# Performance work log

Hardware: AMD Instinct MI355X
Metric: run time of the kernel (lower is better)

The kernel has to match this reference:

```python
import jax, jax.numpy as jnp
import numpy as np
from jax import lax

# ---- constants mirroring Prediction.__init__ kwargs ----
INP = 608
NUM_CLASSES = 20
ALPHA, BETA = 1.0, 0.5
OBJ_T, CONF_T, LOC_T = 0.6, 0.05, 0.5
NMS_T, SIZE_T, SIGMA = 0.1, 0.0, 0.5
TOP_K = 8
M_CAND = 256          # fixed-size candidate cap for jit-compatible NMS
NEG = -1e9            # sentinel for masked scores
ANCHORS = [[(116, 90), (156, 198), (373, 326)],
           [(30, 61), (62, 45), (59, 119)],
           [(10, 13), (16, 30), (33, 23)]]


def _decode(pred, anchors):
    """pred: (B, A, G, G, 6+C) raw level output -> decoded flat tensors."""
    B, A, G, _, C = pred.shape
    stride = INP // G
    xy = jax.nn.sigmoid(pred[..., 0:2])
    g = jnp.arange(G, dtype=pred.dtype)
    gx, gy = jnp.meshgrid(g, g)                      # gx[i,j]=j, gy[i,j]=i (np.meshgrid 'xy')
    off = jnp.stack([gx, gy], axis=-1)[None, None]   # (1,1,G,G,2)
    xy = ALPHA * xy - 0.5 * (ALPHA - 1.0) + off
    anc = jnp.asarray(anchors, dtype=pred.dtype) / stride  # (A,2) scaled to grid units
    wh = jnp.exp(pred[..., 2:4]) * anc[None, :, None, None, :]
    box = jnp.concatenate([xy, wh], axis=-1) * stride       # back to pixel units
    obj = jax.nn.sigmoid(pred[..., 4])
    loc = jax.nn.sigmoid(pred[..., 5])
    clsp = jax.nn.softmax(pred[..., 6:], axis=-1)
    N = A * G * G
    return (box.reshape(B, N, 4), obj.reshape(B, N),
            loc.reshape(B, N), clsp.reshape(B, N, NUM_CLASSES))


def _soft_nms(boxes, s0, cls):
    """Per-image Gaussian soft-NMS (class-aware), +1 pixel IoU convention as in bbox_iou.
    boxes: (M,4) xyxy, s0: (M,) scores (NEG for invalid), cls: (M,) int. Returns kept mask."""
    M = s0.shape[0]

    def step(carry, _):
        s, kept = carry
        j = jnp.argmax(s)
        do = s[j] >= NMS_T
        kept = kept | ((jnp.arange(M) == j) & do)
        bj = boxes[j]
        ix1 = jnp.maximum(bj[0], boxes[:, 0]); iy1 = jnp.maximum(bj[1], boxes[:, 1])
        ix2 = jnp.minimum(bj[2], boxes[:, 2]); iy2 = jnp.minimum(bj[3], boxes[:, 3])
        inter = jnp.maximum(ix2 - ix1 + 1.0, 0.0) * jnp.maximum(iy2 - iy1 + 1.0, 0.0)
        a1 = (bj[2] - bj[0] + 1.0) * (bj[3] - bj[1] + 1.0)
        a2 = (boxes[:, 2] - boxes[:, 0] + 1.0) * (boxes[:, 3] - boxes[:, 1] + 1.0)
        iou = inter / (a1 + a2 - inter + 1e-16)
        decay = jnp.exp(-(iou * iou) / SIGMA)
        s_new = jnp.where(cls == cls[j], s * decay, s).at[j].set(NEG)
        s = jnp.where(do, s_new, s)
        return (s, kept), None

    (_, kept), _ = lax.scan(step, (s0, jnp.zeros(M, dtype=bool)), None, length=M)
    return kept


def _forward(pred_l0, pred_l1, pred_l2):
    parts = [_decode(p, a) for p, a in zip([pred_l0, pred_l1, pred_l2], ANCHORS)]
    box = jnp.concatenate([p[0] for p in parts], axis=1)   # (B,N,4) xywh
    obj = jnp.concatenate([p[1] for p in parts], axis=1)
    loc = jnp.concatenate([p[2] for p in parts], axis=1)
    clsp = jnp.concatenate([p[3] for p in parts], axis=1)

    cx, cy, w, h = box[..., 0], box[..., 1], box[..., 2], box[..., 3]
    x1 = jnp.clip(cx - w / 2, 0.0, INP); y1 = jnp.clip(cy - h / 2, 0.0, INP)
    x2 = jnp.clip(cx + w / 2, 0.0, INP); y2 = jnp.clip(cy + h / 2, 0.0, INP)
    boxes = jnp.stack([x1, y1, x2, y2], axis=-1)            # (B,N,4) xyxy, clamped

    cls_conf = jnp.max(clsp, axis=-1)
    cls_id = jnp.argmax(clsp, axis=-1)
    area = (x2 - x1) * (y2 - y1)
    valid = ((obj >= OBJ_T) & (area >= INP * INP * SIZE_T)
             & (obj * cls_conf >= CONF_T) & (loc >= LOC_T))
    score = (obj * cls_conf) ** BETA * loc ** (1.0 - BETA)
    masked = jnp.where(valid, score, NEG)

    # fixed-size candidate set per image (descending-score sort + cap)
    vals, idx = lax.top_k(masked, M_CAND)                   # (B,M)
    cboxes = jnp.take_along_axis(boxes, idx[..., None], axis=1)
    ccls = jnp.take_along_axis(cls_id, idx, axis=1)
    s0 = jnp.where(vals > NEG / 2, vals, NEG)

    kept = jax.vmap(_soft_nms)(cboxes, s0, ccls)            # (B,M) bool

    # keep_top_k: top_k among kept, ranked by ORIGINAL (pre-decay) score
    fscore = jnp.where(kept, vals, NEG)
    fvals, fidx = lax.top_k(fscore, TOP_K)                  # (B,TOP_K)
    fboxes = jnp.take_along_axis(cboxes, fidx[..., None], axis=1)
    fcls = jnp.take_along_axis(ccls, fidx, axis=1)
    row = jnp.concatenate([fboxes, fvals[..., None],
                           fcls[..., None].astype(fboxes.dtype)], axis=-1)  # (B,K,6)
    ok = fvals > NEG / 2
    return jnp.where(ok[..., None], row, 0.0)


def setup_inputs() -> dict:
    key = jax.random.key(0)
    k0, k1, k2 = jax.random.split(key, 3)
    return {
        "pred_l0": jax.random.normal(k0, (64, 3, 19, 19, 26), dtype=jnp.float32),
        "pred_l1": jax.random.normal(k1, (64, 3, 38, 38, 26), dtype=jnp.float32),
        "pred_l2": jax.random.normal(k2, (64, 3, 76, 76, 26), dtype=jnp.float32),
    }


def reference(pred_l0, pred_l1, pred_l2):
    return _forward(pred_l0, pred_l1, pred_l2)
```

## Files before the change

kernel.cpp:

```cpp
#include <hip/hip_runtime.h>
#include <climits>

constexpr int kB  = 64;
constexpr int kG0 = 19, kG1 = 38, kG2 = 76;
constexpr int kN0 = 3 * kG0 * kG0;
constexpr int kN1 = 3 * kG1 * kG1;
constexpr int kN2 = 3 * kG2 * kG2;
constexpr int kN  = kN0 + kN1 + kN2;
constexpr int kNP = kN + 1;
constexpr int kM  = 256;
constexpr int kTopK = 8;
constexpr float kNEG = -1e9f;

constexpr int kT0 = 5, kT1 = 17, kT2 = 68;
constexpr int kTilesPerImg = kT0 + kT1 + kT2;
constexpr int kGridScore = 1920;
constexpr int kTilesPerBlk = 3;

__constant__ float c_anchors[3][3][2] = {
    {{116.f, 90.f}, {156.f, 198.f}, {373.f, 326.f}},
    {{30.f, 61.f},  {62.f, 45.f},   {59.f, 119.f}},
    {{10.f, 13.f},  {16.f, 30.f},   {33.f, 23.f}},
};

__device__ __forceinline__ float fexpf(float x) { return __expf(x); }
__device__ __forceinline__ float frcpf(float x) { return __builtin_amdgcn_rcpf(x); }
__device__ __forceinline__ float fsigm(float x) { return frcpf(1.0f + __expf(-x)); }

__device__ __forceinline__ float2 nt_load_f2(const float2* p) {
  unsigned long long v = __builtin_nontemporal_load((const unsigned long long*)p);
  union { unsigned long long u; float2 f; } c; c.u = v; return c.f;
}

__device__ __forceinline__ unsigned score_to_key(float s) {
  unsigned fb = __float_as_uint(s);
  unsigned m = (fb & 0x80000000u) ? 0xFFFFFFFFu : 0x80000000u;
  return fb ^ m;
}
__device__ __forceinline__ float key_to_score(unsigned k) {
  unsigned fb = (k & 0x80000000u) ? (k ^ 0x80000000u) : ~k;
  return __uint_as_float(fb);
}

__device__ __forceinline__ const float* cell_ptr(
    const float* p0, const float* p1, const float* p2, int b, int n,
    int& lvl, int& a, int& gi, int& gj, float& stride) {
  const float* src; int G, m;
  if (n < kN0)            { src = p0; G = kG0; lvl = 0; m = n;             stride = 32.f; }
  else if (n < kN0 + kN1) { src = p1; G = kG1; lvl = 1; m = n - kN0;       stride = 16.f; }
  else                    { src = p2; G = kG2; lvl = 2; m = n - kN0 - kN1; stride = 8.f; }
  int gg = G * G;
  a = m / gg;
  int r = m - a * gg;
  gi = r / G;
  gj = r - gi * G;
  return src + (size_t)((((b * 3 + a) * G + gi) * G + gj)) * 26;
}

__device__ __forceinline__ void waveArgmax(float& v, int& i) {
  #pragma unroll
  for (int off = 1; off < 64; off <<= 1) {
    float ov = __shfl_xor(v, off);
    int oi = __shfl_xor(i, off);
    if (ov > v || (ov == v && oi < i)) { v = ov; i = oi; }
  }
}
__device__ __forceinline__ float waveMax(float v) {
  #pragma unroll
  for (int off = 1; off < 64; off <<= 1) v = fmaxf(v, __shfl_xor(v, off));
  return v;
}
__device__ __forceinline__ float sel4f(const float a[4], int q) {
  float r = a[0];
  r = (q == 1) ? a[1] : r;
  r = (q == 2) ? a[2] : r;
  r = (q == 3) ? a[3] : r;
  return r;
}
__device__ __forceinline__ int sel4i(const int a[4], int q) {
  int r = a[0];
  r = (q == 1) ? a[1] : r;
  r = (q == 2) ? a[2] : r;
  r = (q == 3) ? a[3] : r;
  return r;
}

__global__ __launch_bounds__(256) void score_kernel(
    const float* __restrict__ p0, const float* __restrict__ p1, const float* __restrict__ p2,
    unsigned* __restrict__ keys)
{
  __shared__ float2 lds2[2][256 * 13];

  int t = threadIdx.x;

  const float2* g2[kTilesPerBlk]; int nc[kTilesPerBlk], n0[kTilesPerBlk], bb[kTilesPerBlk];
  #pragma unroll
  for (int j = 0; j < kTilesPerBlk; ++j) {
    int tileId = (int)blockIdx.x + j * kGridScore;
    int b = tileId / kTilesPerImg;
    int r = tileId - b * kTilesPerImg;
    const float* slab; int NL, lvlOff, tile;
    if (r < kT0)            { slab = p0; NL = kN0; lvlOff = 0;         tile = r; }
    else if (r < kT0 + kT1) { slab = p1; NL = kN1; lvlOff = kN0;       tile = r - kT0; }
    else                    { slab = p2; NL = kN2; lvlOff = kN0 + kN1; tile = r - kT0 - kT1; }
    int cellBase = tile * 256;
    nc[j] = min(256, NL - cellBase);
    g2[j] = (const float2*)(slab + ((size_t)b * NL + cellBase) * 26);
    n0[j] = lvlOff + cellBase;
    bb[j] = b;
  }

  float2 nxt[13];

  {
    int tot = nc[0] * 13;
    #pragma unroll
    for (int k = 0; k < 13; ++k) {
      int i = t + k * 256;
      if (i < tot) nxt[k] = nt_load_f2(g2[0] + i);
    }
    #pragma unroll
    for (int k = 0; k < 13; ++k) {
      int i = t + k * 256;
      if (i < tot) lds2[0][i] = nxt[k];
    }
  }

  #pragma unroll
  for (int j = 0; j < kTilesPerBlk; ++j) {
    __syncthreads();

    int totN = 0;
    if (j + 1 < kTilesPerBlk) {
      totN = nc[j + 1] * 13;
      #pragma unroll
      for (int k = 0; k < 13; ++k) {
        int i = t + k * 256;
        if (i < totN) nxt[k] = nt_load_f2(g2[j + 1] + i);
      }
    }

    int curNc = nc[j], curN0 = n0[j], curB = bb[j];
    const float2* bufp = &lds2[j & 1][0];
    if (t < curNc) {
      const float2* c2 = &bufp[t * 13];
      float2 ol = c2[2];
      float obj = fsigm(ol.x);
      float loc = fsigm(ol.y);
      float tch[20];
      #pragma unroll
      for (int q = 0; q < 10; ++q) { float2 v = c2[3 + q]; tch[2*q] = v.x; tch[2*q+1] = v.y; }
      float lm = tch[0];
      #pragma unroll
      for (int c = 1; c < 20; ++c) lm = fmaxf(lm, tch[c]);
      float se = 0.f;
      #pragma unroll
      for (int c = 0; c < 20; ++c) se += fexpf(tch[c] - lm);
      float cls_conf = frcpf(se);
      float conf = obj * cls_conf;
      float masked = (obj >= 0.6f && loc >= 0.5f && conf >= 0.05f)
                     ? sqrtf(conf) * sqrtf(loc) : kNEG;
      keys[(size_t)curB * kNP + curN0 + t] = score_to_key(masked);
    }

    if (j + 1 < kTilesPerBlk) {
      float2* dst = &lds2[(j + 1) & 1][0];
      #pragma unroll
      for (int k = 0; k < 13; ++k) {
        int i = t + k * 256;
        if (i < totN) dst[i] = nxt[k];
      }
    }
  }
}

__device__ __forceinline__ void findThresholdBin(
    const int* hist, int NB, int needed,
    int& outB, int& outCumAbove, int& outTotal,
    int* shWave, int* shOut)
{
  int tid = threadIdx.x, lane = tid & 63, w = tid >> 6;
  if (tid == 0) { shOut[0] = -1; shOut[1] = 0; }
  int ipt = (NB + 511) / 512;
  int base = tid * ipt;
  int csum = 0;
  for (int i = 0; i < ipt; ++i) { int bn = base + i; if (bn < NB) csum += hist[bn]; }
  int v = csum;
  #pragma unroll
  for (int off = 1; off < 64; off <<= 1) {
    int tv = __shfl_down(v, off);
    if (lane + off < 64) v += tv;
  }
  if (lane == 0) shWave[w] = v;
  __syncthreads();
  int above = 0, total = 0;
  #pragma unroll
  for (int q = 0; q < 8; ++q) {
    int wt = shWave[q];
    total += wt;
    if (q > w) above += wt;
  }
  int S = v + above;
  if (S >= needed && S - csum < needed) {
    int running = S - csum;
    for (int i = ipt - 1; i >= 0; --i) {
      int bn = base + i; if (bn >= NB) continue;
      int c = hist[bn];
      if (running + c >= needed) { shOut[0] = bn; shOut[1] = running; break; }
      running += c;
    }
  }
  __syncthreads();
  outB = shOut[0]; outCumAbove = shOut[1]; outTotal = total;
  __syncthreads();
}

constexpr int kNV4 = kN / 4;
constexpr int kTail = kN - kNV4*4;

__global__ __launch_bounds__(512) void select_nms_kernel(
    const unsigned* __restrict__ keys,
    const float* __restrict__ p0, const float* __restrict__ p1, const float* __restrict__ p2,
    float* __restrict__ out)
{
  int b = blockIdx.x, tid = threadIdx.x;
  const unsigned* kk = keys + (size_t)b * kNP;
  const uint4* kk4 = (const uint4*)kk;
  const unsigned keyNEG = score_to_key(kNEG);

  __shared__ int hist[4096];
  __shared__ int eqBuf[1024];
  __shared__ int shWave[8], shOut[2];
  __shared__ unsigned sT;
  __shared__ int sCgt;
  __shared__ int ciL[kM];
  __shared__ unsigned ckL[kM];

  for (int i = tid; i < 4096; i += 512) hist[i] = 0;
  __syncthreads();
  for (int x = tid; x < kNV4; x += 512) {
    uint4 v = kk4[x];
    if (v.x >= 0x80000000u) atomicAdd(&hist[v.x >> 20], 1);
    if (v.y >= 0x80000000u) atomicAdd(&hist[v.y >> 20], 1);
    if (v.z >= 0x80000000u) atomicAdd(&hist[v.z >> 20], 1);
    if (v.w >= 0x80000000u) atomicAdd(&hist[v.w >> 20], 1);
  }
  if (tid < kTail) {
    unsigned k = kk[kNV4 * 4 + tid];
    if (k >= 0x80000000u) atomicAdd(&hist[k >> 20], 1);
  }
  __syncthreads();
  int B, cumAbove1, total1;
  findThresholdBin(hist, 4096, kM, B, cumAbove1, total1, shWave, shOut);

  if (total1 < kM) {
    if (tid == 0) { sT = keyNEG; sCgt = total1; }
    __syncthreads();
  } else {
    int needed2 = kM - cumAbove1;
    for (int i = tid; i < 4096; i += 512) hist[i] = 0;
    __syncthreads();
    for (int x = tid; x < kNV4; x += 512) {
      uint4 v = kk4[x];
      if ((int)(v.x >> 20) == B) atomicAdd(&hist[(v.x >> 8) & 0xFFF], 1);
      if ((int)(v.y >> 20) == B) atomicAdd(&hist[(v.y >> 8) & 0xFFF], 1);
      if ((int)(v.z >> 20) == B) atomicAdd(&hist[(v.z >> 8) & 0xFFF], 1);
      if ((int)(v.w >> 20) == B) atomicAdd(&hist[(v.w >> 8) & 0xFFF], 1);
    }
    if (tid < kTail) {
      unsigned k = kk[kNV4 * 4 + tid];
      if ((int)(k >> 20) == B) atomicAdd(&hist[(k >> 8) & 0xFFF], 1);
    }
    __syncthreads();
    int B2, cumAbove2, total2;
    findThresholdBin(hist, 4096, needed2, B2, cumAbove2, total2, shWave, shOut);
    int prefix24 = (B << 12) | B2;
    int needed3 = needed2 - cumAbove2;

    for (int i = tid; i < 256; i += 512) hist[i] = 0;
    __syncthreads();
    for (int x = tid; x < kNV4; x += 512) {
      uint4 v = kk4[x];
      if ((int)(v.x >> 8) == prefix24) atomicAdd(&hist[v.x & 0xFF], 1);
      if ((int)(v.y >> 8) == prefix24) atomicAdd(&hist[v.y & 0xFF], 1);
      if ((int)(v.z >> 8) == prefix24) atomicAdd(&hist[v.z & 0xFF], 1);
      if ((int)(v.w >> 8) == prefix24) atomicAdd(&hist[v.w & 0xFF], 1);
    }
    if (tid < kTail) {
      unsigned k = kk[kNV4 * 4 + tid];
      if ((int)(k >> 8) == prefix24) atomicAdd(&hist[k & 0xFF], 1);
    }
    __syncthreads();
    int B3, cumAbove3, total3;
    findThresholdBin(hist, 256, needed3, B3, cumAbove3, total3, shWave, shOut);
    if (tid == 0) {
      sT = ((unsigned)prefix24 << 8) | (unsigned)B3;
      sCgt = cumAbove1 + cumAbove2 + cumAbove3;
    }
    __syncthreads();
  }

  unsigned T = sT;
  int cgt = sCgt;

  __shared__ int sCnt, eqCnt;
  if (tid == 0) { sCnt = 0; eqCnt = 0; }
  __syncthreads();
  for (int x = tid; x < kNV4; x += 512) {
    uint4 v = kk4[x];
    int i4 = x * 4;
    unsigned kv[4] = {v.x, v.y, v.z, v.w};
    #pragma unroll
    for (int e = 0; e < 4; ++e) {
      unsigned k = kv[e];
      if (k > T) {
        int p = atomicAdd(&sCnt, 1);
        ciL[p] = i4 + e; ckL[p] = k;
      } else if (k == T && T != keyNEG) {
        int p = atomicAdd(&eqCnt, 1); if (p < 1024) eqBuf[p] = i4 + e;
      }
    }
  }
  if (tid < kTail) {
    int x = kNV4 * 4 + tid;
    unsigned k = kk[x];
    if (k > T) {
      int p = atomicAdd(&sCnt, 1);
      ciL[p] = x; ckL[p] = k;
    } else if (k == T && T != keyNEG) {
      int p = atomicAdd(&eqCnt, 1); if (p < 1024) eqBuf[p] = x;
    }
  }
  __syncthreads();

  int needed = kM - cgt;
  if (T == keyNEG) {
    if (tid >= cgt && tid < kM) { ciL[tid] = -1; ckL[tid] = keyNEG; }
  } else {
    int ce = min(eqCnt, 1024);
    if (ce == needed) {
      if (tid < needed) { ciL[cgt + tid] = eqBuf[tid]; ckL[cgt + tid] = T; }
    } else if (tid == 0) {
      for (int q = 0; q < needed; ++q) {
        int mv = INT_MAX, mp = 0;
        for (int x = 0; x < ce; ++x) if (eqBuf[x] < mv) { mv = eqBuf[x]; mp = x; }
        ciL[cgt + q] = mv; ckL[cgt + q] = T; eqBuf[mp] = INT_MAX;
      }
    }
  }
  __syncthreads();

  if (tid >= 64) return;
  int lane = tid;

  float x1[4], y1[4], x2[4], y2[4], val[4], s[4];
  int cls[4];
  bool kept[4];

  #pragma unroll
  for (int q = 0; q < 4; ++q) {
    int slot = q * 64 + lane;
    int n = ciL[slot];
    float sc = key_to_score(ckL[slot]);
    kept[q] = false;
    x1[q] = y1[q] = x2[q] = y2[q] = 0.f;
    cls[q] = 0; val[q] = sc; s[q] = sc;
    if (n >= 0) {
      int lvl, a, gi, gj; float stride;
      const float* p = cell_ptr(p0, p1, p2, b, n, lvl, a, gi, gj, stride);
      const float2* r2 = (const float2*)p;
      float2 c01 = r2[0], c23 = r2[1];
      float cx = (fsigm(c01.x) + (float)gj) * stride;
      float cy = (fsigm(c01.y) + (float)gi) * stride;
      float w = fexpf(c23.x) * c_anchors[lvl][a][0];
      float h = fexpf(c23.y) * c_anchors[lvl][a][1];
      x1[q] = fminf(fmaxf(cx - 0.5f * w, 0.f), 608.f);
      y1[q] = fminf(fmaxf(cy - 0.5f * h, 0.f), 608.f);
      x2[q] = fminf(fmaxf(cx + 0.5f * w, 0.f), 608.f);
      y2[q] = fminf(fmaxf(cy + 0.5f * h, 0.f), 608.f);
      float lm = -3.4e38f; int mc = 0;
      #pragma unroll
      for (int j = 3; j < 13; ++j) {
        float2 v = r2[j];
        int c0 = 2 * (j - 3);
        if (v.x > lm) { lm = v.x; mc = c0; }
        if (v.y > lm) { lm = v.y; mc = c0 + 1; }
      }
      cls[q] = mc;
    }
  }

  float top8[8];
  #pragma unroll
  for (int i = 0; i < 8; ++i) top8[i] = kNEG;
  int keptCount = 0;

  for (int it = 0; it < kM; ++it) {
    float bv = s[0]; int bq = 0;
    #pragma unroll
    for (int q = 1; q < 4; ++q) if (s[q] > bv) { bv = s[q]; bq = q; }
    int bi = bq * 64 + lane;
    waveArgmax(bv, bi);
    if (bv < 0.1f) break;

    int wlane = bi & 63, wq = bi >> 6;
    float jx1 = __shfl(sel4f(x1, wq), wlane);
    float jy1 = __shfl(sel4f(y1, wq), wlane);
    float jx2 = __shfl(sel4f(x2, wq), wlane);
    float jy2 = __shfl(sel4f(y2, wq), wlane);
    float jval = __shfl(sel4f(val, wq), wlane);
    int   cj  = __shfl(sel4i(cls, wq), wlane);

    float a1 = (jx2 - jx1 + 1.0f) * (jy2 - jy1 + 1.0f);
    #pragma unroll
    for (int q = 0; q < 4; ++q) {
      if (cls[q] == cj) {
        float ix1 = fmaxf(jx1, x1[q]), iy1 = fmaxf(jy1, y1[q]);
        float ix2 = fminf(jx2, x2[q]), iy2 = fminf(jy2, y2[q]);
        float inter = fmaxf(ix2 - ix1 + 1.0f, 0.0f) * fmaxf(iy2 - iy1 + 1.0f, 0.0f);
        float a2 = (x2[q] - x1[q] + 1.0f) * (y2[q] - y1[q] + 1.0f);
        float iou = inter / (a1 + a2 - inter + 1e-16f);
        s[q] *= fexpf(-(iou * iou) * 2.0f);
      }
      if (bi == q * 64 + lane) { kept[q] = true; s[q] = kNEG; }
    }

    float v = jval;
    #pragma unroll
    for (int i = 0; i < 8; ++i) { float m = fmaxf(top8[i], v); v = fminf(top8[i], v); top8[i] = m; }
    ++keptCount;
    if (keptCount >= kTopK) {
      float am = kNEG;
      #pragma unroll
      for (int q = 0; q < 4; ++q) if (s[q] >= 0.1f) am = fmaxf(am, val[q]);
      am = waveMax(am);
      if (am < top8[7]) break;
    }
  }

  float f[4];
  #pragma unroll
  for (int q = 0; q < 4; ++q) f[q] = kept[q] ? val[q] : kNEG;
  for (int k = 0; k < kTopK; ++k) {
    float bv = f[0]; int bq = 0;
    #pragma unroll
    for (int q = 1; q < 4; ++q) if (f[q] > bv) { bv = f[q]; bq = q; }
    int bi = bq * 64 + lane;
    waveArgmax(bv, bi);
    int wlane = bi & 63, wq = bi >> 6;
    if (lane == wlane) {
      float* o = out + (size_t)(b * kTopK + k) * 6;
      if (bv > kNEG * 0.5f) {
        o[0] = sel4f(x1, wq); o[1] = sel4f(y1, wq);
        o[2] = sel4f(x2, wq); o[3] = sel4f(y2, wq);
        o[4] = sel4f(val, wq); o[5] = (float)sel4i(cls, wq);
      } else {
        o[0] = 0.f; o[1] = 0.f; o[2] = 0.f; o[3] = 0.f; o[4] = 0.f; o[5] = 0.f;
      }
    }
    #pragma unroll
    for (int q = 0; q < 4; ++q) if (bi == q * 64 + lane) f[q] = kNEG;
  }
}

extern "C" void kernel_launch(void* const* d_in, const int* in_sizes, int n_in,
                              void* d_out, int out_size, void* d_ws, size_t ws_size,
                              hipStream_t stream) {
  const float* p0 = (const float*)d_in[0];
  const float* p1 = (const float*)d_in[1];
  const float* p2 = (const float*)d_in[2];
  float* out = (float*)d_out;

  unsigned* keys = (unsigned*)d_ws;

  score_kernel<<<kGridScore, 256, 0, stream>>>(p0, p1, p2, keys);
  select_nms_kernel<<<kB, 512, 0, stream>>>(keys, p0, p1, p2, out);
}
```

Measured before the change: 226.3 us.

## Fuse score and select/NMS kernels via last-block-done atomic counters

Result: slower. 665.4 us (+194.0%).

```diff
diff --git a/kernel.cpp b/kernel.cpp
--- a/kernel.cpp
+++ b/kernel.cpp
@@ -16,6 +16,9 @@
 constexpr int kTilesPerImg = kT0 + kT1 + kT2;
 constexpr int kGridScore = 1920;
 constexpr int kTilesPerBlk = 3;
+
+constexpr int kNV4 = kN / 4;
+constexpr int kTail = kN - kNV4 * 4;
 
 __constant__ float c_anchors[3][3][2] = {
     {{116.f, 90.f}, {156.f, 198.f}, {373.f, 326.f}},
@@ -85,11 +88,56 @@
   return r;
 }
 
-__global__ __launch_bounds__(256) void score_kernel(
+__device__ __forceinline__ void findThresholdBin256(
+    const int* hist, int NB, int needed,
+    int& outB, int& outCumAbove, int& outTotal,
+    int* shWave, int* shOut)
+{
+  int tid = threadIdx.x, lane = tid & 63, w = tid >> 6;
+  if (tid == 0) { shOut[0] = -1; shOut[1] = 0; }
+  int ipt = (NB + 255) / 256;
+  int base = tid * ipt;
+  int csum = 0;
+  for (int i = 0; i < ipt; ++i) { int bn = base + i; if (bn < NB) csum += hist[bn]; }
+  int v = csum;
+  #pragma unroll
+  for (int off = 1; off < 64; off <<= 1) {
+    int tv = __shfl_down(v, off);
+    if (lane + off < 64) v += tv;
+  }
+  if (lane == 0) shWave[w] = v;
+  __syncthreads();
+  int above = 0, total = 0;
+  #pragma unroll
+  for (int q = 0; q < 4; ++q) {
+    int wt = shWave[q];
+    total += wt;
+    if (q > w) above += wt;
+  }
+  int S = v + above;
+  if (S >= needed && S - csum < needed) {
+    int running = S - csum;
+    for (int i = ipt - 1; i >= 0; --i) {
+      int bn = base + i; if (bn >= NB) continue;
+      int c = hist[bn];
+      if (running + c >= needed) { shOut[0] = bn; shOut[1] = running; break; }
+      running += c;
+    }
+  }
+  __syncthreads();
+  outB = shOut[0]; outCumAbove = shOut[1]; outTotal = total;
+  __syncthreads();
+}
+
+__global__ __launch_bounds__(256) void fused_kernel(
     const float* __restrict__ p0, const float* __restrict__ p1, const float* __restrict__ p2,
-    unsigned* __restrict__ keys)
+    unsigned* __restrict__ keys, int* __restrict__ done, float* __restrict__ out)
 {
-  __shared__ float2 lds2[2][256 * 13];
+  __shared__ float2 smem2[2][256 * 13];
+  __shared__ int shWave[4], shOut[2];
+  __shared__ unsigned sT;
+  __shared__ int sCgt, sCnt, sEqCnt;
+  __shared__ int sFlags[kTilesPerBlk], sNF;
 
   int t = threadIdx.x;
 
@@ -110,356 +158,325 @@
     bb[j] = b;
   }
 
-  float2 nxt[13];
-
   {
-    int tot = nc[0] * 13;
-    #pragma unroll
-    for (int k = 0; k < 13; ++k) {
-      int i = t + k * 256;
-      if (i < tot) nxt[k] = nt_load_f2(g2[0] + i);
-    }
-    #pragma unroll
-    for (int k = 0; k < 13; ++k) {
-      int i = t + k * 256;
-      if (i < tot) lds2[0][i] = nxt[k];
-    }
-  }
-
-  #pragma unroll
-  for (int j = 0; j < kTilesPerBlk; ++j) {
-    __syncthreads();
-
-    int totN = 0;
-    if (j + 1 < kTilesPerBlk) {
-      totN = nc[j + 1] * 13;
+    float2 nxt[13];
+    {
+      int tot = nc[0] * 13;
       #pragma unroll
       for (int k = 0; k < 13; ++k) {
         int i = t + k * 256;
-        if (i < totN) nxt[k] = nt_load_f2(g2[j + 1] + i);
-      }
-    }
-
-    int curNc = nc[j], curN0 = n0[j], curB = bb[j];
-    const float2* bufp = &lds2[j & 1][0];
-    if (t < curNc) {
-      const float2* c2 = &bufp[t * 13];
-      float2 ol = c2[2];
-      float obj = fsigm(ol.x);
-      float loc = fsigm(ol.y);
-      float tch[20];
-      #pragma unroll
-      for (int q = 0; q < 10; ++q) { float2 v = c2[3 + q]; tch[2*q] = v.x; tch[2*q+1] = v.y; }
-      float lm = tch[0];
-      #pragma unroll
-      for (int c = 1; c < 20; ++c) lm = fmaxf(lm, tch[c]);
-      float se = 0.f;
-      #pragma unroll
-      for (int c = 0; c < 20; ++c) se += fexpf(tch[c] - lm);
-      float cls_conf = frcpf(se);
-      float conf = obj * cls_conf;
-      float masked = (obj >= 0.6f && loc >= 0.5f && conf >= 0.05f)
-                     ? sqrtf(conf) * sqrtf(loc) : kNEG;
-      keys[(size_t)curB * kNP + curN0 + t] = score_to_key(masked);
-    }
-
-    if (j + 1 < kTilesPerBlk) {
-      float2* dst = &lds2[(j + 1) & 1][0];
+        if (i < tot) nxt[k] = nt_load_f2(g2[0] + i);
+      }
       #pragma unroll
       for (int k = 0; k < 13; ++k) {
         int i = t + k * 256;
-        if (i < totN) dst[i] = nxt[k];
-      }
-    }
-  }
-}
-
-__device__ __forceinline__ void findThresholdBin(
-    const int* hist, int NB, int needed,
-    int& outB, int& outCumAbove, int& outTotal,
-    int* shWave, int* shOut)
-{
-  int tid = threadIdx.x, lane = tid & 63, w = tid >> 6;
-  if (tid == 0) { shOut[0] = -1; shOut[1] = 0; }
-  int ipt = (NB + 511) / 512;
-  int base = tid * ipt;
-  int csum = 0;
-  for (int i = 0; i < ipt; ++i) { int bn = base + i; if (bn < NB) csum += hist[bn]; }
-  int v = csum;
-  #pragma unroll
-  for (int off = 1; off < 64; off <<= 1) {
-    int tv = __shfl_down(v, off);
-    if (lane + off < 64) v += tv;
-  }
-  if (lane == 0) shWave[w] = v;
+        if (i < tot) smem2[0][i] = nxt[k];
+      }
+    }
+
+    #pragma unroll
+    for (int j = 0; j < kTilesPerBlk; ++j) {
+      __syncthreads();
+
+      int totN = 0;
+      if (j + 1 < kTilesPerBlk) {
+        totN = nc[j + 1] * 13;
+        #pragma unroll
+        for (int k = 0; k < 13; ++k) {
+          int i = t + k * 256;
+          if (i < totN) nxt[k] = nt_load_f2(g2[j + 1] + i);
+        }
+      }
+
+      int curNc = nc[j], curN0 = n0[j], curB = bb[j];
+      const float2* bufp = &smem2[j & 1][0];
+      if (t < curNc) {
+        const float2* c2 = &bufp[t * 13];
+        float2 ol = c2[2];
+        float obj = fsigm(ol.x);
+        float loc = fsigm(ol.y);
+        float tch[20];
+        #pragma unroll
+        for (int q = 0; q < 10; ++q) { float2 v = c2[3 + q]; tch[2*q] = v.x; tch[2*q+1] = v.y; }
+        float lm = tch[0];
+        #pragma unroll
+        for (int c = 1; c < 20; ++c) lm = fmaxf(lm, tch[c]);
+        float se = 0.f;
+        #pragma unroll
+        for (int c = 0; c < 20; ++c) se += fexpf(tch[c] - lm);
+        float cls_conf = frcpf(se);
+        float conf = obj * cls_conf;
+        float masked = (obj >= 0.6f && loc >= 0.5f && conf >= 0.05f)
+                       ? sqrtf(conf) * sqrtf(loc) : kNEG;
+        keys[(size_t)curB * kNP + curN0 + t] = score_to_key(masked);
+      }
+
+      if (j + 1 < kTilesPerBlk) {
+        float2* dst = &smem2[(j + 1) & 1][0];
+        #pragma unroll
+        for (int k = 0; k < 13; ++k) {
+          int i = t + k * 256;
+          if (i < totN) dst[i] = nxt[k];
+        }
+      }
+    }
+  }
+
   __syncthreads();
-  int above = 0, total = 0;
-  #pragma unroll
-  for (int q = 0; q < 8; ++q) {
-    int wt = shWave[q];
-    total += wt;
-    if (q > w) above += wt;
-  }
-  int S = v + above;
-  if (S >= needed && S - csum < needed) {
-    int running = S - csum;
-    for (int i = ipt - 1; i >= 0; --i) {
-      int bn = base + i; if (bn >= NB) continue;
-      int c = hist[bn];
-      if (running + c >= needed) { shOut[0] = bn; shOut[1] = running; break; }
-      running += c;
-    }
+  __threadfence();
+  if (t == 0) {
+    int nf = 0;
+    #pragma unroll
+    for (int j = 0; j < kTilesPerBlk; ++j) {
+      int old = atomicAdd(&done[bb[j]], 1);
+      if (old == kTilesPerImg - 1) sFlags[nf++] = bb[j];
+    }
+    sNF = nf;
   }
   __syncthreads();
-  outB = shOut[0]; outCumAbove = shOut[1]; outTotal = total;
-  __syncthreads();
-}
-
-constexpr int kNV4 = kN / 4;
-constexpr int kTail = kN - kNV4*4;
-
-__global__ __launch_bounds__(512) void select_nms_kernel(
-    const unsigned* __restrict__ keys,
-    const float* __restrict__ p0, const float* __restrict__ p1, const float* __restrict__ p2,
-    float* __restrict__ out)
-{
-  int b = blockIdx.x, tid = threadIdx.x;
-  const unsigned* kk = keys + (size_t)b * kNP;
-  const uint4* kk4 = (const uint4*)kk;
+  int nFlag = sNF;
+  if (nFlag == 0) return;
+
+  int* hist = (int*)&smem2[0][0];
+  int* eqBuf = hist + 4096;
+  int* ciL = eqBuf + 1024;
+  unsigned* ckL = (unsigned*)(ciL + 256);
+
   const unsigned keyNEG = score_to_key(kNEG);
 
-  __shared__ int hist[4096];
-  __shared__ int eqBuf[1024];
-  __shared__ int shWave[8], shOut[2];
-  __shared__ unsigned sT;
-  __shared__ int sCgt;
-  __shared__ int ciL[kM];
-  __shared__ unsigned ckL[kM];
-
-  for (int i = tid; i < 4096; i += 512) hist[i] = 0;
-  __syncthreads();
-  for (int x = tid; x < kNV4; x += 512) {
-    uint4 v = kk4[x];
-    if (v.x >= 0x80000000u) atomicAdd(&hist[v.x >> 20], 1);
-    if (v.y >= 0x80000000u) atomicAdd(&hist[v.y >> 20], 1);
-    if (v.z >= 0x80000000u) atomicAdd(&hist[v.z >> 20], 1);
-    if (v.w >= 0x80000000u) atomicAdd(&hist[v.w >> 20], 1);
-  }
-  if (tid < kTail) {
-    unsigned k = kk[kNV4 * 4 + tid];
-    if (k >= 0x80000000u) atomicAdd(&hist[k >> 20], 1);
-  }
-  __syncthreads();
-  int B, cumAbove1, total1;
-  findThresholdBin(hist, 4096, kM, B, cumAbove1, total1, shWave, shOut);
-
-  if (total1 < kM) {
-    if (tid == 0) { sT = keyNEG; sCgt = total1; }
-    __syncthreads();
-  } else {
-    int needed2 = kM - cumAbove1;
-    for (int i = tid; i < 4096; i += 512) hist[i] = 0;
-    __syncthreads();
-    for (int x = tid; x < kNV4; x += 512) {
+  for (int f = 0; f < nFlag; ++f) {
+    int b = sFlags[f];
+    __threadfence();
+    __syncthreads();
+
+    const unsigned* kk = keys + (size_t)b * kNP;
+    const uint4* kk4 = (const uint4*)kk;
+
+    for (int i = t; i < 4096; i += 256) hist[i] = 0;
+    __syncthreads();
+    for (int x = t; x < kNV4; x += 256) {
       uint4 v = kk4[x];
-      if ((int)(v.x >> 20) == B) atomicAdd(&hist[(v.x >> 8) & 0xFFF], 1);
-      if ((int)(v.y >> 20) == B) atomicAdd(&hist[(v.y >> 8) & 0xFFF], 1);
-      if ((int)(v.z >> 20) == B) atomicAdd(&hist[(v.z >> 8) & 0xFFF], 1);
-      if ((int)(v.w >> 20) == B) atomicAdd(&hist[(v.w >> 8) & 0xFFF], 1);
-    }
-    if (tid < kTail) {
-      unsigned k = kk[kNV4 * 4 + tid];
-      if ((int)(k >> 20) == B) atomicAdd(&hist[(k >> 8) & 0xFFF], 1);
-    }
-    __syncthreads();
-    int B2, cumAbove2, total2;
-    findThresholdBin(hist, 4096, needed2, B2, cumAbove2, total2, shWave, shOut);
-    int prefix24 = (B << 12) | B2;
-    int needed3 = needed2 - cumAbove2;
-
-    for (int i = tid; i < 256; i += 512) hist[i] = 0;
-    __syncthreads();
-    for (int x = tid; x < kNV4; x += 512) {
+      if (v.x >= 0x80000000u) atomicAdd(&hist[v.x >> 20], 1);
+      if (v.y >= 0x80000000u) atomicAdd(&hist[v.y >> 20], 1);
+      if (v.z >= 0x80000000u) atomicAdd(&hist[v.z >> 20], 1);
+      if (v.w >= 0x80000000u) atomicAdd(&hist[v.w >> 20], 1);
+    }
+    if (t < kTail) {
+      unsigned k = kk[kNV4 * 4 + t];
+      if (k >= 0x80000000u) atomicAdd(&hist[k >> 20], 1);
+    }
+    __syncthreads();
+    int B, cumAbove1, total1;
+    findThresholdBin256(hist, 4096, kM, B, cumAbove1, total1, shWave, shOut);
+
+    if (total1 < kM) {
+      if (t == 0) { sT = keyNEG; sCgt = total1; }
+      __syncthreads();
+    } else {
+      int needed2 = kM - cumAbove1;
+      for (int i = t; i < 4096; i += 256) hist[i] = 0;
+      __syncthreads();
+      for (int x = t; x < kNV4; x += 256) {
+        uint4 v = kk4[x];
+        if ((int)(v.x >> 20) == B) atomicAdd(&hist[(v.x >> 8) & 0xFFF], 1);
+        if ((int)(v.y >> 20) == B) atomicAdd(&hist[(v.y >> 8) & 0xFFF], 1);
+        if ((int)(v.z >> 20) == B) atomicAdd(&hist[(v.z >> 8) & 0xFFF], 1);
+        if ((int)(v.w >> 20) == B) atomicAdd(&hist[(v.w >> 8) & 0xFFF], 1);
+      }
+      if (t < kTail) {
+        unsigned k = kk[kNV4 * 4 + t];
+        if ((int)(k >> 20) == B) atomicAdd(&hist[(k >> 8) & 0xFFF], 1);
+      }
+      __syncthreads();
+      int B2, cumAbove2, total2;
+      findThresholdBin256(hist, 4096, needed2, B2, cumAbove2, total2, shWave, shOut);
+      int prefix24 = (B << 12) | B2;
+      int needed3 = needed2 - cumAbove2;
+
+      for (int i = t; i < 256; i += 256) hist[i] = 0;
+      __syncthreads();
+      for (int x = t; x < kNV4; x += 256) {
+        uint4 v = kk4[x];
+        if ((int)(v.x >> 8) == prefix24) atomicAdd(&hist[v.x & 0xFF], 1);
+        if ((int)(v.y >> 8) == prefix24) atomicAdd(&hist[v.y & 0xFF], 1);
+        if ((int)(v.z >> 8) == prefix24) atomicAdd(&hist[v.z & 0xFF], 1);
+        if ((int)(v.w >> 8) == prefix24) atomicAdd(&hist[v.w & 0xFF], 1);
+      }
+      if (t < kTail) {
+        unsigned k = kk[kNV4 * 4 + t];
+        if ((int)(k >> 8) == prefix24) atomicAdd(&hist[k & 0xFF], 1);
+      }
+      __syncthreads();
+      int B3, cumAbove3, total3;
+      findThresholdBin256(hist, 256, needed3, B3, cumAbove3, total3, shWave, shOut);
+      if (t == 0) {
+        sT = ((unsigned)prefix24 << 8) | (unsigned)B3;
+        sCgt = cumAbove1 + cumAbove2 + cumAbove3;
+      }
+      __syncthreads();
+    }
+
+    unsigned T = sT;
+    int cgt = sCgt;
+
+    if (t == 0) { sCnt = 0; sEqCnt = 0; }
+    __syncthreads();
+    for (int x = t; x < kNV4; x += 256) {
       uint4 v = kk4[x];
-      if ((int)(v.x >> 8) == prefix24) atomicAdd(&hist[v.x & 0xFF], 1);
-      if ((int)(v.y >> 8) == prefix24) atomicAdd(&hist[v.y & 0xFF], 1);
-      if ((int)(v.z >> 8) == prefix24) atomicAdd(&hist[v.z & 0xFF], 1);
-      if ((int)(v.w >> 8) == prefix24) atomicAdd(&hist[v.w & 0xFF], 1);
-    }
-    if (tid < kTail) {
-      unsigned k = kk[kNV4 * 4 + tid];
-      if ((int)(k >> 8) == prefix24) atomicAdd(&hist[k & 0xFF], 1);
-    }
-    __syncthreads();
-    int B3, cumAbove3, total3;
-    findThresholdBin(hist, 256, needed3, B3, cumAbove3, total3, shWave, shOut);
-    if (tid == 0) {
-      sT = ((unsigned)prefix24 << 8) | (unsigned)B3;
-      sCgt = cumAbove1 + cumAbove2 + cumAbove3;
-    }
-    __syncthreads();
-  }
-
-  unsigned T = sT;
-  int cgt = sCgt;
-
-  __shared__ int sCnt, eqCnt;
-  if (tid == 0) { sCnt = 0; eqCnt = 0; }
-  __syncthreads();
-  for (int x = tid; x < kNV4; x += 512) {
-    uint4 v = kk4[x];
-    int i4 = x * 4;
-    unsigned kv[4] = {v.x, v.y, v.z, v.w};
-    #pragma unroll
-    for (int e = 0; e < 4; ++e) {
-      unsigned k = kv[e];
+      int i4 = x * 4;
+      unsigned kv[4] = {v.x, v.y, v.z, v.w};
+      #pragma unroll
+      for (int e = 0; e < 4; ++e) {
+        unsigned k = kv[e];
+        if (k > T) {
+          int p = atomicAdd(&sCnt, 1);
+          ciL[p] = i4 + e; ckL[p] = k;
+        } else if (k == T && T != keyNEG) {
+          int p = atomicAdd(&sEqCnt, 1); if (p < 1024) eqBuf[p] = i4 + e;
+        }
+      }
+    }
+    if (t < kTail) {
+      int x = kNV4 * 4 + t;
+      unsigned k = kk[x];
       if (k > T) {
         int p = atomicAdd(&sCnt, 1);
-        ciL[p] = i4 + e; ckL[p] = k;
+        ciL[p] = x; ckL[p] = k;
       } else if (k == T && T != keyNEG) {
-        int p = atomicAdd(&eqCnt, 1); if (p < 1024) eqBuf[p] = i4 + e;
-      }
-    }
-  }
-  if (tid < kTail) {
-    int x = kNV4 * 4 + tid;
-    unsigned k = kk[x];
-    if (k > T) {
-      int p = atomicAdd(&sCnt, 1);
-      ciL[p] = x; ckL[p] = k;
-    } else if (k == T && T != keyNEG) {
-      int p = atomicAdd(&eqCnt, 1); if (p < 1024) eqBuf[p] = x;
-    }
-  }
-  __syncthreads();
-
-  int needed = kM - cgt;
-  if (T == keyNEG) {
-    if (tid >= cgt && tid < kM) { ciL[tid] = -1; ckL[tid] = keyNEG; }
-  } else {
-    int ce = min(eqCnt, 1024);
-    if (ce == needed) {
-      if (tid < needed) { ciL[cgt + tid] = eqBuf[tid]; ckL[cgt + tid] = T; }
-    } else if (tid == 0) {
-      for (int q = 0; q < needed; ++q) {
-        int mv = INT_MAX, mp = 0;
-        for (int x = 0; x < ce; ++x) if (eqBuf[x] < mv) { mv = eqBuf[x]; mp = x; }
-        ciL[cgt + q] = mv; ckL[cgt + q] = T; eqBuf[mp] = INT_MAX;
-      }
-    }
-  }
-  __syncthreads();
-
-  if (tid >= 64) return;
-  int lane = tid;
-
-  float x1[4], y1[4], x2[4], y2[4], val[4], s[4];
-  int cls[4];
-  bool kept[4];
-
-  #pragma unroll
-  for (int q = 0; q < 4; ++q) {
-    int slot = q * 64 + lane;
-    int n = ciL[slot];
-    float sc = key_to_score(ckL[slot]);
-    kept[q] = false;
-    x1[q] = y1[q] = x2[q] = y2[q] = 0.f;
-    cls[q] = 0; val[q] = sc; s[q] = sc;
-    if (n >= 0) {
-      int lvl, a, gi, gj; float stride;
-      const float* p = cell_ptr(p0, p1, p2, b, n, lvl, a, gi, gj, stride);
-      const float2* r2 = (const float2*)p;
-      float2 c01 = r2[0], c23 = r2[1];
-      float cx = (fsigm(c01.x) + (float)gj) * stride;
-      float cy = (fsigm(c01.y) + (float)gi) * stride;
-      float w = fexpf(c23.x) * c_anchors[lvl][a][0];
-      float h = fexpf(c23.y) * c_anchors[lvl][a][1];
-      x1[q] = fminf(fmaxf(cx - 0.5f * w, 0.f), 608.f);
-      y1[q] = fminf(fmaxf(cy - 0.5f * h, 0.f), 608.f);
-      x2[q] = fminf(fmaxf(cx + 0.5f * w, 0.f), 608.f);
-      y2[q] = fminf(fmaxf(cy + 0.5f * h, 0.f), 608.f);
-      float lm = -3.4e38f; int mc = 0;
-      #pragma unroll
-      for (int j = 3; j < 13; ++j) {
-        float2 v = r2[j];
-        int c0 = 2 * (j - 3);
-        if (v.x > lm) { lm = v.x; mc = c0; }
-        if (v.y > lm) { lm = v.y; mc = c0 + 1; }
-      }
-      cls[q] = mc;
-    }
-  }
-
-  float top8[8];
-  #pragma unroll
-  for (int i = 0; i < 8; ++i) top8[i] = kNEG;
-  int keptCount = 0;
-
-  for (int it = 0; it < kM; ++it) {
-    float bv = s[0]; int bq = 0;
-    #pragma unroll
-    for (int q = 1; q < 4; ++q) if (s[q] > bv) { bv = s[q]; bq = q; }
-    int bi = bq * 64 + lane;
-    waveArgmax(bv, bi);
-    if (bv < 0.1f) break;
-
-    int wlane = bi & 63, wq = bi >> 6;
-    float jx1 = __shfl(sel4f(x1, wq), wlane);
-    float jy1 = __shfl(sel4f(y1, wq), wlane);
-    float jx2 = __shfl(sel4f(x2, wq), wlane);
-    float jy2 = __shfl(sel4f(y2, wq), wlane);
-    float jval = __shfl(sel4f(val, wq), wlane);
-    int   cj  = __shfl(sel4i(cls, wq), wlane);
-
-    float a1 = (jx2 - jx1 + 1.0f) * (jy2 - jy1 + 1.0f);
-    #pragma unroll
-    for (int q = 0; q < 4; ++q) {
-      if (cls[q] == cj) {
-        float ix1 = fmaxf(jx1, x1[q]), iy1 = fmaxf(jy1, y1[q]);
-        float ix2 = fminf(jx2, x2[q]), iy2 = fminf(jy2, y2[q]);
-        float inter = fmaxf(ix2 - ix1 + 1.0f, 0.0f) * fmaxf(iy2 - iy1 + 1.0f, 0.0f);
-        float a2 = (x2[q] - x1[q] + 1.0f) * (y2[q] - y1[q] + 1.0f);
-        float iou = inter / (a1 + a2 - inter + 1e-16f);
-        s[q] *= fexpf(-(iou * iou) * 2.0f);
-      }
-      if (bi == q * 64 + lane) { kept[q] = true; s[q] = kNEG; }
-    }
-
-    float v = jval;
-    #pragma unroll
-    for (int i = 0; i < 8; ++i) { float m = fmaxf(top8[i], v); v = fminf(top8[i], v); top8[i] = m; }
-    ++keptCount;
-    if (keptCount >= kTopK) {
-      float am = kNEG;
-      #pragma unroll
-      for (int q = 0; q < 4; ++q) if (s[q] >= 0.1f) am = fmaxf(am, val[q]);
-      am = waveMax(am);
-      if (am < top8[7]) break;
-    }
-  }
-
-  float f[4];
-  #pragma unroll
-  for (int q = 0; q < 4; ++q) f[q] = kept[q] ? val[q] : kNEG;
-  for (int k = 0; k < kTopK; ++k) {
-    float bv = f[0]; int bq = 0;
-    #pragma unroll
-    for (int q = 1; q < 4; ++q) if (f[q] > bv) { bv = f[q]; bq = q; }
-    int bi = bq * 64 + lane;
-    waveArgmax(bv, bi);
-    int wlane = bi & 63, wq = bi >> 6;
-    if (lane == wlane) {
-      float* o = out + (size_t)(b * kTopK + k) * 6;
-      if (bv > kNEG * 0.5f) {
-        o[0] = sel4f(x1, wq); o[1] = sel4f(y1, wq);
-        o[2] = sel4f(x2, wq); o[3] = sel4f(y2, wq);
-        o[4] = sel4f(val, wq); o[5] = (float)sel4i(cls, wq);
-      } else {
-        o[0] = 0.f; o[1] = 0.f; o[2] = 0.f; o[3] = 0.f; o[4] = 0.f; o[5] = 0.f;
-      }
-    }
-    #pragma unroll
-    for (int q = 0; q < 4; ++q) if (bi == q * 64 + lane) f[q] = kNEG;
+        int p = atomicAdd(&sEqCnt, 1); if (p < 1024) eqBuf[p] = x;
+      }
+    }
+    __syncthreads();
+
+    int needed = kM - cgt;
+    if (T == keyNEG) {
+      if (t >= cgt && t < kM) { ciL[t] = -1; ckL[t] = keyNEG; }
+    } else {
+      int ce = min(sEqCnt, 1024);
+      if (ce == needed) {
+        if (t < needed) { ciL[cgt + t] = eqBuf[t]; ckL[cgt + t] = T; }
+      } else if (t == 0) {
+        for (int q = 0; q < needed; ++q) {
+          int mv = INT_MAX, mp = 0;
+          for (int x = 0; x < ce; ++x) if (eqBuf[x] < mv) { mv = eqBuf[x]; mp = x; }
+          ciL[cgt + q] = mv; ckL[cgt + q] = T; eqBuf[mp] = INT_MAX;
+        }
+      }
+    }
+    __syncthreads();
+
+    if (t < 64) {
+      int lane = t;
+      float x1[4], y1[4], x2[4], y2[4], val[4], s[4];
+      int cls[4];
+      bool kept[4];
+
+      #pragma unroll
+      for (int q = 0; q < 4; ++q) {
+        int slot = q * 64 + lane;
+        int n = ciL[slot];
+        float sc = key_to_score(ckL[slot]);
+        kept[q] = false;
+        x1[q] = y1[q] = x2[q] = y2[q] = 0.f;
+        cls[q] = 0; val[q] = sc; s[q] = sc;
+        if (n >= 0) {
+          int lvl, a, gi, gj; float stride;
+          const float* p = cell_ptr(p0, p1, p2, b, n, lvl, a, gi, gj, stride);
+          const float2* r2 = (const float2*)p;
+          float2 c01 = r2[0], c23 = r2[1];
+          float cx = (fsigm(c01.x) + (float)gj) * stride;
+          float cy = (fsigm(c01.y) + (float)gi) * stride;
+          float w = fexpf(c23.x) * c_anchors[lvl][a][0];
+          float h = fexpf(c23.y) * c_anchors[lvl][a][1];
+          x1[q] = fminf(fmaxf(cx - 0.5f * w, 0.f), 608.f);
+          y1[q] = fminf(fmaxf(cy - 0.5f * h, 0.f), 608.f);
+          x2[q] = fminf(fmaxf(cx + 0.5f * w, 0.f), 608.f);
+          y2[q] = fminf(fmaxf(cy + 0.5f * h, 0.f), 608.f);
+          float lm = -3.4e38f; int mc = 0;
+          #pragma unroll
+          for (int j = 3; j < 13; ++j) {
+            float2 v = r2[j];
+            int c0 = 2 * (j - 3);
+            if (v.x > lm) { lm = v.x; mc = c0; }
+            if (v.y > lm) { lm = v.y; mc = c0 + 1; }
+          }
+          cls[q] = mc;
+        }
+      }
+
+      float top8[8];
+      #pragma unroll
+      for (int i = 0; i < 8; ++i) top8[i] = kNEG;
+      int keptCount = 0;
+
+      for (int it = 0; it < kM; ++it) {
+        float bv = s[0]; int bq = 0;
+        #pragma unroll
+        for (int q = 1; q < 4; ++q) if (s[q] > bv) { bv = s[q]; bq = q; }
+        int bi = bq * 64 + lane;
+        waveArgmax(bv, bi);
+        if (bv < 0.1f) break;
+
+        int wlane = bi & 63, wq = bi >> 6;
+        float jx1 = __shfl(sel4f(x1, wq), wlane);
+        float jy1 = __shfl(sel4f(y1, wq), wlane);
+        float jx2 = __shfl(sel4f(x2, wq), wlane);
+        float jy2 = __shfl(sel4f(y2, wq), wlane);
+        float jval = __shfl(sel4f(val, wq), wlane);
+        int   cj  = __shfl(sel4i(cls, wq), wlane);
+
+        float a1 = (jx2 - jx1 + 1.0f) * (jy2 - jy1 + 1.0f);
+        #pragma unroll
+        for (int q = 0; q < 4; ++q) {
+          if (cls[q] == cj) {
+            float ix1 = fmaxf(jx1, x1[q]), iy1 = fmaxf(jy1, y1[q]);
+            float ix2 = fminf(jx2, x2[q]), iy2 = fminf(jy2, y2[q]);
+            float inter = fmaxf(ix2 - ix1 + 1.0f, 0.0f) * fmaxf(iy2 - iy1 + 1.0f, 0.0f);
+            float a2 = (x2[q] - x1[q] + 1.0f) * (y2[q] - y1[q] + 1.0f);
+            float iou = inter / (a1 + a2 - inter + 1e-16f);
+            s[q] *= fexpf(-(iou * iou) * 2.0f);
+          }
+          if (bi == q * 64 + lane) { kept[q] = true; s[q] = kNEG; }
+        }
+
+        float v = jval;
+        #pragma unroll
+        for (int i = 0; i < 8; ++i) { float m = fmaxf(top8[i], v); v = fminf(top8[i], v); top8[i] = m; }
+        ++keptCount;
+        if (keptCount >= kTopK) {
+          float am = kNEG;
+          #pragma unroll
+          for (int q = 0; q < 4; ++q) if (s[q] >= 0.1f) am = fmaxf(am, val[q]);
+          am = waveMax(am);
+          if (am < top8[7]) break;
+        }
+      }
+
+      float fsc[4];
+      #pragma unroll
+      for (int q = 0; q < 4; ++q) fsc[q] = kept[q] ? val[q] : kNEG;
+      for (int k = 0; k < kTopK; ++k) {
+        float bv = fsc[0]; int bq = 0;
+        #pragma unroll
+        for (int q = 1; q < 4; ++q) if (fsc[q] > bv) { bv = fsc[q]; bq = q; }
+        int bi = bq * 64 + lane;
+        waveArgmax(bv, bi);
+        int wlane = bi & 63, wq = bi >> 6;
+        if (lane == wlane) {
+          float* o = out + (size_t)(b * kTopK + k) * 6;
+          if (bv > kNEG * 0.5f) {
+            o[0] = sel4f(x1, wq); o[1] = sel4f(y1, wq);
+            o[2] = sel4f(x2, wq); o[3] = sel4f(y2, wq);
+            o[4] = sel4f(val, wq); o[5] = (float)sel4i(cls, wq);
+          } else {
+            o[0] = 0.f; o[1] = 0.f; o[2] = 0.f; o[3] = 0.f; o[4] = 0.f; o[5] = 0.f;
+          }
+        }
+        #pragma unroll
+        for (int q = 0; q < 4; ++q) if (bi == q * 64 + lane) fsc[q] = kNEG;
+      }
+    }
+    __syncthreads();
   }
 }
 
@@ -472,7 +489,8 @@
   float* out = (float*)d_out;
 
   unsigned* keys = (unsigned*)d_ws;
-
-  score_kernel<<<kGridScore, 256, 0, stream>>>(p0, p1, p2, keys);
-  select_nms_kernel<<<kB, 512, 0, stream>>>(keys, p0, p1, p2, out);
-}
+  int* done = (int*)(keys + (size_t)kB * kNP);
+
+  hipMemsetAsync(done, 0, kB * sizeof(int), stream);
+  fused_kernel<<<kGridScore, 256, 0, stream>>>(p0, p1, p2, keys, done, out);
+}
```
